# Kernel optimization log

Hardware: AMD Instinct MI355X
Metric: run time of the kernel (lower is better)

## Reference

```python
import jax, jax.numpy as jnp
import numpy as np

N_NODES = 10000
N_EDGES = 160000
D = 256
L = 2
EPS = 1e-5


def setup_inputs() -> dict:
    key = jax.random.key(0)
    ks = jax.random.split(key, 12)
    s = 0.05  # weight init scale to keep activations tame
    return {
        "node_h": jax.random.normal(ks[0], (N_NODES, D), jnp.float32),
        "edge_h": jax.random.normal(ks[1], (N_EDGES, D), jnp.float32),
        "src": jax.random.randint(ks[2], (N_EDGES,), 0, N_NODES, jnp.int32),
        "dst": jax.random.randint(ks[3], (N_EDGES,), 0, N_NODES, jnp.int32),
        "Kw": jax.random.normal(ks[4], (L, 2 * D, D), jnp.float32) * s,
        "Kb": jnp.zeros((L, D), jnp.float32),
        "Vw": jax.random.normal(ks[5], (L, 2 * D, D), jnp.float32) * s,
        "Vb": jnp.zeros((L, D), jnp.float32),
        "Qw": jax.random.normal(ks[6], (L, D, D), jnp.float32) * s,
        "Qb": jnp.zeros((L, D), jnp.float32),
        "Ww": jax.random.normal(ks[7], (L, 2 * D, D), jnp.float32) * s,
        "Wb": jnp.zeros((L, D), jnp.float32),
        "Ew": jax.random.normal(ks[8], (L, 3 * D, D), jnp.float32) * s,
        "Eb": jnp.zeros((L, D), jnp.float32),
        "ln_g": jnp.ones((D,), jnp.float32),
        "ln_b": jnp.zeros((D,), jnp.float32),
    }


def _layernorm(x, g, b):
    mu = jnp.mean(x, axis=-1, keepdims=True)
    var = jnp.mean(jnp.square(x - mu), axis=-1, keepdims=True)
    return (x - mu) * jax.lax.rsqrt(var + EPS) * g + b


def _hypergraph_layer(h_n, h_e, src, dst, Kw, Kb, Vw, Vb, Qw, Qb, Ww, Wb, Ew, Eb):
    n = h_n.shape[0]
    src_h = h_n[src]                                   # [E, D] gather
    msg = jnp.concatenate([src_h * h_e, src_h], axis=1)  # [E, 2D]
    Q = h_n @ Qw + Qb                                  # [N, D]
    K = msg @ Kw + Kb                                  # [E, D]
    V = msg @ Vw + Vb                                  # [E, D]
    alpha = Q[dst] * K                                 # v_mul_e -> [E, D]
    # edge_softmax: per-destination-node, per-feature softmax over edges
    m = jax.ops.segment_max(alpha, dst, num_segments=n)
    e = jnp.exp(alpha - m[dst])
    z = jax.ops.segment_sum(e, dst, num_segments=n)
    a = e / z[dst]
    agg = jax.ops.segment_sum(a * V, dst, num_segments=n)  # sum aggregation [N, D]
    h_n_new = jnp.concatenate([agg, h_n], axis=1) @ Ww + Wb
    h_e_new = jnp.concatenate([h_n_new[src], h_n_new[dst], h_e], axis=1) @ Ew + Eb
    return h_n_new, h_e_new


def reference(node_h, edge_h, src, dst, Kw, Kb, Vw, Vb, Qw, Qb, Ww, Wb, Ew, Eb, ln_g, ln_b):
    h_n, h_e = node_h, edge_h
    for l in range(L):  # small fixed layer count
        h_n, h_e = _hypergraph_layer(h_n, h_e, src, dst,
                                     Kw[l], Kb[l], Vw[l], Vb[l], Qw[l], Qb[l],
                                     Ww[l], Wb[l], Ew[l], Eb[l])
        # relu -> layernorm; dropout is identity in eval mode
        h_n = _layernorm(jax.nn.relu(h_n), ln_g, ln_b)
        h_e = _layernorm(jax.nn.relu(h_e), ln_g, ln_b)
    return h_n, h_e
```

## Files before the change

### kernel.cpp

```cpp
#include <hip/hip_runtime.h>

#define NN 10000
#define NE 160000
#define DD 256
#define LEPS 1e-5f

typedef __attribute__((ext_vector_type(8))) short short8v;
typedef __attribute__((ext_vector_type(4))) float floatx4;
typedef unsigned short US;

static __device__ __forceinline__ US f2bf(float f){
  unsigned u = __builtin_bit_cast(unsigned, f);
  u += 0x7FFFu + ((u >> 16) & 1u);
  return (US)(u >> 16);
}
static __device__ __forceinline__ float bf2f(US s){
  unsigned u = ((unsigned)s) << 16;
  return __builtin_bit_cast(float, u);
}
template<typename T>
static __device__ __forceinline__ void ld8(const T* p, float* o){
  if constexpr (sizeof(T) == 2) {
    union { US h[8]; uint4 q; } u;
    u.q = *(const uint4*)p;
#pragma unroll
    for (int j = 0; j < 8; ++j) o[j] = bf2f(u.h[j]);
  } else {
    float4 a = *(const float4*)p; float4 b = *(const float4*)(p + 4);
    o[0]=a.x; o[1]=a.y; o[2]=a.z; o[3]=a.w; o[4]=b.x; o[5]=b.y; o[6]=b.z; o[7]=b.w;
  }
}
template<typename OT>
static __device__ __forceinline__ void st1(OT* p, float v){
  if constexpr (sizeof(OT) == 2) *p = (OT)f2bf(v); else *p = (OT)v;
}

#define AOFF_Q  0
#define AOFF_K1 (32*2048)
#define AOFF_K2 (64*2048)
#define AOFF_V1 (96*2048)
#define AOFF_V2 (128*2048)
#define AOFF_W  (160*2048)
#define AOFF_E1 (224*2048)
#define AOFF_E2 (256*2048)
#define AOFF_E3 (288*2048)
__global__ void pack_all_k(const float* __restrict__ Qw, const float* __restrict__ Kw,
                           const float* __restrict__ Vw, const float* __restrict__ Ww,
                           const float* __restrict__ Ew, US* __restrict__ arena){
  int i = blockIdx.x * 256 + threadIdx.x;
  int g = i >> 8, n = i & 255;
  const float* src; int row0;
  if      (g <  32){ src = Qw; row0 = g*8; }
  else if (g <  64){ src = Kw; row0 = (g-32)*8; }
  else if (g <  96){ src = Kw; row0 = 256 + (g-64)*8; }
  else if (g < 128){ src = Vw; row0 = (g-96)*8; }
  else if (g < 160){ src = Vw; row0 = 256 + (g-128)*8; }
  else if (g < 224){ src = Ww; row0 = (g-160)*8; }
  else if (g < 256){ src = Ew; row0 = (g-224)*8; }
  else if (g < 288){ src = Ew; row0 = 256 + (g-256)*8; }
  else             { src = Ew; row0 = 512 + (g-288)*8; }
  union { US h[8]; uint4 q; } pk;
#pragma unroll
  for (int j = 0; j < 8; ++j) pk.h[j] = f2bf(src[(size_t)(row0 + j)*DD + n]);
  *(uint4*)(arena + (size_t)g*2048 + n*8) = pk.q;
}

template<typename AT, typename OT>
__global__ __launch_bounds__(256, 2)
void gemm_nmulti_k(const AT* __restrict__ p0,
                   const US* bp0, const float* b0, OT* o0,
                   const US* bp1, const float* b1, OT* o1,
                   const US* bp2, const float* b2, OT* o2, int M)
{
  const US* Bp  = (blockIdx.y == 0) ? bp0 : (blockIdx.y == 1 ? bp1 : bp2);
  const float* bias = (blockIdx.y == 0) ? b0 : (blockIdx.y == 1 ? b1 : b2);
  OT* out = (blockIdx.y == 0) ? o0 : (blockIdx.y == 1 ? o1 : o2);
  __shared__ __align__(16) US Alds[64][40];
  __shared__ __align__(16) US Blds[8192];
  const int tid  = threadIdx.x;
  const int lane = tid & 63;
  const int wav  = tid >> 6;
  const int bm   = blockIdx.x * 64;

  floatx4 acc[4][4];
#pragma unroll
  for (int i = 0; i < 4; ++i)
#pragma unroll
    for (int j = 0; j < 4; ++j) acc[i][j] = (floatx4){0.f,0.f,0.f,0.f};

  const int ar = tid >> 2;
  const int ak = (tid & 3) << 3;
  int grow = bm + ar; if (grow > M - 1) grow = M - 1;
  const AT* rA = p0 + (size_t)grow * DD;
  const int rq = lane >> 4;
  const int cl = lane & 15;

  for (int k0 = 0; k0 < 256; k0 += 32) {
    float av[8]; ld8(rA + k0 + ak, av);
    union { US h[8]; uint4 q; } pk;
#pragma unroll
    for (int j = 0; j < 8; ++j) pk.h[j] = f2bf(av[j]);
    *(uint4*)&Alds[ar][ak] = pk.q;

    const uint4* bsrc = (const uint4*)(Bp + (size_t)(k0 >> 3) * 2048);
    uint4* bdst = (uint4*)Blds;
#pragma unroll
    for (int u = 0; u < 4; ++u) bdst[tid + u*256] = bsrc[tid + u*256];
    __syncthreads();

    short8v af[4], bfr[4];
#pragma unroll
    for (int i = 0; i < 4; ++i) af[i] = *(const short8v*)&Alds[i*16 + cl][rq*8];
#pragma unroll
    for (int j = 0; j < 4; ++j) bfr[j] = *(const short8v*)&Blds[(size_t)(rq*256 + wav*64 + j*16 + cl) * 8];
#pragma unroll
    for (int i = 0; i < 4; ++i)
#pragma unroll
      for (int j = 0; j < 4; ++j)
        acc[i][j] = __builtin_amdgcn_mfma_f32_16x16x32_bf16(af[i], bfr[j], acc[i][j], 0, 0, 0);
    __syncthreads();
  }

#pragma unroll
  for (int i = 0; i < 4; ++i)
#pragma unroll
    for (int r = 0; r < 4; ++r) {
      int gm = bm + i*16 + rq*4 + r;
      if (gm < M) {
#pragma unroll
        for (int j = 0; j < 4; ++j) {
          int n = wav*64 + j*16 + cl;
          float b = bias ? bias[n] : 0.f;
          st1(out + (size_t)gm*DD + n, acc[i][j][r] + b);
        }
      }
    }
}

template<typename AT, typename OT>
__global__ __launch_bounds__(256, 2)
void gemm_w_k(const float* __restrict__ p0, const AT* __restrict__ p1,
              const US* __restrict__ Bp, const float* __restrict__ bias,
              const float* __restrict__ lg, const float* __restrict__ lb,
              float* __restrict__ Craw, OT* __restrict__ Cln, int M)
{
  __shared__ __align__(16) US Alds[64][40];
  __shared__ __align__(16) US Blds[8192];
  __shared__ float S1[4][64], S2[4][64];
  const int tid  = threadIdx.x;
  const int lane = tid & 63;
  const int wav  = tid >> 6;
  const int bm   = blockIdx.x * 64;

  floatx4 acc[4][4];
#pragma unroll
  for (int i = 0; i < 4; ++i)
#pragma unroll
    for (int j = 0; j < 4; ++j) acc[i][j] = (floatx4){0.f,0.f,0.f,0.f};

  const int ar = tid >> 2;
  const int ak = (tid & 3) << 3;
  int grow = bm + ar; if (grow > M - 1) grow = M - 1;
  const float* rA = p0 + (size_t)grow * DD;
  const AT*    rB = p1 + (size_t)grow * DD;
  const int rq = lane >> 4;
  const int cl = lane & 15;

  for (int k0 = 0; k0 < 512; k0 += 32) {
    const int kk = k0 + ak;
    float av[8];
    if (kk < DD) ld8(rA + kk, av); else ld8(rB + kk - DD, av);
    union { US h[8]; uint4 q; } pk;
#pragma unroll
    for (int j = 0; j < 8; ++j) pk.h[j] = f2bf(av[j]);
    *(uint4*)&Alds[ar][ak] = pk.q;

    const uint4* bsrc = (const uint4*)(Bp + (size_t)(k0 >> 3) * 2048);
    uint4* bdst = (uint4*)Blds;
#pragma unroll
    for (int u = 0; u < 4; ++u) bdst[tid + u*256] = bsrc[tid + u*256];
    __syncthreads();

    short8v af[4], bfr[4];
#pragma unroll
    for (int i = 0; i < 4; ++i) af[i] = *(const short8v*)&Alds[i*16 + cl][rq*8];
#pragma unroll
    for (int j = 0; j < 4; ++j) bfr[j] = *(const short8v*)&Blds[(size_t)(rq*256 + wav*64 + j*16 + cl) * 8];
#pragma unroll
    for (int i = 0; i < 4; ++i)
#pragma unroll
      for (int j = 0; j < 4; ++j)
        acc[i][j] = __builtin_amdgcn_mfma_f32_16x16x32_bf16(af[i], bfr[j], acc[i][j], 0, 0, 0);
    __syncthreads();
  }

#pragma unroll
  for (int i = 0; i < 4; ++i)
#pragma unroll
    for (int j = 0; j < 4; ++j) {
      int n = wav*64 + j*16 + cl;
      float bs = bias[n];
#pragma unroll
      for (int r = 0; r < 4; ++r) {
        int gm = bm + i*16 + rq*4 + r;
        float val = acc[i][j][r] + bs;
        if (gm < M) Craw[(size_t)gm*DD + n] = val;
        acc[i][j][r] = fmaxf(val, 0.f);
      }
    }
#pragma unroll
  for (int i = 0; i < 4; ++i)
#pragma unroll
    for (int r = 0; r < 4; ++r) {
      float s1 = 0.f, s2 = 0.f;
#pragma unroll
      for (int j = 0; j < 4; ++j){ float v = acc[i][j][r]; s1 += v; s2 += v*v; }
#pragma unroll
      for (int o = 1; o < 16; o <<= 1){ s1 += __shfl_xor(s1, o, 64); s2 += __shfl_xor(s2, o, 64); }
      if (cl == 0){ S1[wav][i*16 + rq*4 + r] = s1; S2[wav][i*16 + rq*4 + r] = s2; }
    }
  __syncthreads();
#pragma unroll
  for (int i = 0; i < 4; ++i)
#pragma unroll
    for (int r = 0; r < 4; ++r) {
      int rr = i*16 + rq*4 + r;
      float t1 = S1[0][rr] + S1[1][rr] + S1[2][rr] + S1[3][rr];
      float t2 = S2[0][rr] + S2[1][rr] + S2[2][rr] + S2[3][rr];
      float mu = t1 * (1.f/256.f);
      float var = t2 * (1.f/256.f) - mu*mu;
      float rs = rsqrtf(fmaxf(var, 0.f) + LEPS);
      int gm = bm + i*16 + rq*4 + r;
      if (gm < M) {
#pragma unroll
        for (int j = 0; j < 4; ++j) {
          int n = wav*64 + j*16 + cl;
          st1(Cln + (size_t)gm*DD + n, (acc[i][j][r] - mu) * rs * lg[n] + lb[n]);
        }
      }
    }
}

template<typename AT>
__global__ __launch_bounds__(256, 2)
void gemm_kve_k(const AT* __restrict__ p0, const AT* __restrict__ p1,
                const int* __restrict__ srcI,
                const US* __restrict__ BpK, const US* __restrict__ BpV,
                const US* __restrict__ KN, const US* __restrict__ VN,
                const int* __restrict__ eperm,
                US* __restrict__ Km, US* __restrict__ Vm, int M)
{
  __shared__ __align__(16) US Alds[64][40];
  __shared__ __align__(16) US BldsK[8192];
  __shared__ __align__(16) US BldsV[8192];
  const int tid  = threadIdx.x;
  const int lane = tid & 63;
  const int wav  = tid >> 6;
  const int bm   = blockIdx.x * 64;

  floatx4 accK[4][4], accV[4][4];
#pragma unroll
  for (int i = 0; i < 4; ++i)
#pragma unroll
    for (int j = 0; j < 4; ++j){ accK[i][j] = (floatx4){0.f,0.f,0.f,0.f}; accV[i][j] = (floatx4){0.f,0.f,0.f,0.f}; }

  const int ar = tid >> 2;
  const int ak = (tid & 3) << 3;
  int grow = bm + ar; if (grow > M - 1) grow = M - 1;
  int s = srcI[grow];
  const AT* rA = p0 + (size_t)s * DD;
  const AT* rB = p1 + (size_t)grow * DD;
  const int rq = lane >> 4;
  const int cl = lane & 15;

  for (int k0 = 0; k0 < 256; k0 += 32) {
    const int kk = k0 + ak;
    float av[8], bv[8];
    ld8(rA + kk, av); ld8(rB + kk, bv);
    union { US h[8]; uint4 q; } pk;
#pragma unroll
    for (int j = 0; j < 8; ++j) pk.h[j] = f2bf(av[j] * bv[j]);
    *(uint4*)&Alds[ar][ak] = pk.q;

    const uint4* bsK = (const uint4*)(BpK + (size_t)(k0 >> 3) * 2048);
    const uint4* bsV = (const uint4*)(BpV + (size_t)(k0 >> 3) * 2048);
    uint4* bdK = (uint4*)BldsK; uint4* bdV = (uint4*)BldsV;
#pragma unroll
    for (int u = 0; u < 4; ++u){ bdK[tid + u*256] = bsK[tid + u*256]; bdV[tid + u*256] = bsV[tid + u*256]; }
    __syncthreads();

    short8v af[4], bK4[4], bV4[4];
#pragma unroll
    for (int i = 0; i < 4; ++i) af[i] = *(const short8v*)&Alds[i*16 + cl][rq*8];
#pragma unroll
    for (int j = 0; j < 4; ++j){
      size_t bi = (size_t)(rq*256 + wav*64 + j*16 + cl) * 8;
      bK4[j] = *(const short8v*)&BldsK[bi];
      bV4[j] = *(const short8v*)&BldsV[bi];
    }
#pragma unroll
    for (int i = 0; i < 4; ++i)
#pragma unroll
      for (int j = 0; j < 4; ++j){
        accK[i][j] = __builtin_amdgcn_mfma_f32_16x16x32_bf16(af[i], bK4[j], accK[i][j], 0, 0, 0);
        accV[i][j] = __builtin_amdgcn_mfma_f32_16x16x32_bf16(af[i], bV4[j], accV[i][j], 0, 0, 0);
      }
    __syncthreads();
  }

#pragma unroll
  for (int i = 0; i < 4; ++i)
#pragma unroll
    for (int r = 0; r < 4; ++r) {
      int gm = bm + i*16 + rq*4 + r;
      if (gm < M) {
        int pg = eperm[gm];
        int sg = srcI[gm];
        const US* kn = KN + (size_t)sg * DD;
        const US* vn = VN + (size_t)sg * DD;
#pragma unroll
        for (int j = 0; j < 4; ++j) {
          int n = wav*64 + j*16 + cl;
          Km[(size_t)pg*DD + n] = f2bf(accK[i][j][r] + bf2f(kn[n]));
          Vm[(size_t)pg*DD + n] = f2bf(accV[i][j][r] + bf2f(vn[n]));
        }
      }
    }
}

template<typename AT, typename OT>
__global__ __launch_bounds__(256, 2)
void gemm_e_k(const AT* __restrict__ he, const int* __restrict__ srcI,
              const int* __restrict__ dstI, const US* __restrict__ Bp,
              const US* __restrict__ EN1, const US* __restrict__ EN2,
              const float* __restrict__ lg, const float* __restrict__ lb,
              OT* __restrict__ Cln, int M)
{
  __shared__ __align__(16) US Alds[64][40];
  __shared__ __align__(16) US Blds[8192];
  __shared__ float S1[4][64], S2[4][64];
  const int tid  = threadIdx.x;
  const int lane = tid & 63;
  const int wav  = tid >> 6;
  const int bm   = blockIdx.x * 64;

  floatx4 acc[4][4];
#pragma unroll
  for (int i = 0; i < 4; ++i)
#pragma unroll
    for (int j = 0; j < 4; ++j) acc[i][j] = (floatx4){0.f,0.f,0.f,0.f};

  const int ar = tid >> 2;
  const int ak = (tid & 3) << 3;
  int grow = bm + ar; if (grow > M - 1) grow = M - 1;
  const AT* rA = he + (size_t)grow * DD;
  const int rq = lane >> 4;
  const int cl = lane & 15;

  for (int k0 = 0; k0 < 256; k0 += 32) {
    float av[8]; ld8(rA + k0 + ak, av);
    union { US h[8]; uint4 q; } pk;
#pragma unroll
    for (int j = 0; j < 8; ++j) pk.h[j] = f2bf(av[j]);
    *(uint4*)&Alds[ar][ak] = pk.q;

    const uint4* bsrc = (const uint4*)(Bp + (size_t)(k0 >> 3) * 2048);
    uint4* bdst = (uint4*)Blds;
#pragma unroll
    for (int u = 0; u < 4; ++u) bdst[tid + u*256] = bsrc[tid + u*256];
    __syncthreads();

    short8v af[4], bfr[4];
#pragma unroll
    for (int i = 0; i < 4; ++i) af[i] = *(const short8v*)&Alds[i*16 + cl][rq*8];
#pragma unroll
    for (int j = 0; j < 4; ++j) bfr[j] = *(const short8v*)&Blds[(size_t)(rq*256 + wav*64 + j*16 + cl) * 8];
#pragma unroll
    for (int i = 0; i < 4; ++i)
#pragma unroll
      for (int j = 0; j < 4; ++j)
        acc[i][j] = __builtin_amdgcn_mfma_f32_16x16x32_bf16(af[i], bfr[j], acc[i][j], 0, 0, 0);
    __syncthreads();
  }

#pragma unroll
  for (int i = 0; i < 4; ++i)
#pragma unroll
    for (int r = 0; r < 4; ++r) {
      int gm = bm + i*16 + rq*4 + r;
      int gmc = (gm < M) ? gm : (M - 1);
      const US* e1 = EN1 + (size_t)srcI[gmc] * DD;
      const US* e2 = EN2 + (size_t)dstI[gmc] * DD;
#pragma unroll
      for (int j = 0; j < 4; ++j) {
        int n = wav*64 + j*16 + cl;
        float val = acc[i][j][r] + bf2f(e1[n]) + bf2f(e2[n]);
        acc[i][j][r] = fmaxf(val, 0.f);
      }
    }
#pragma unroll
  for (int i = 0; i < 4; ++i)
#pragma unroll
    for (int r = 0; r < 4; ++r) {
      float s1 = 0.f, s2 = 0.f;
#pragma unroll
      for (int j = 0; j < 4; ++j){ float v = acc[i][j][r]; s1 += v; s2 += v*v; }
#pragma unroll
      for (int o = 1; o < 16; o <<= 1){ s1 += __shfl_xor(s1, o, 64); s2 += __shfl_xor(s2, o, 64); }
      if (cl == 0){ S1[wav][i*16 + rq*4 + r] = s1; S2[wav][i*16 + rq*4 + r] = s2; }
    }
  __syncthreads();
#pragma unroll
  for (int i = 0; i < 4; ++i)
#pragma unroll
    for (int r = 0; r < 4; ++r) {
      int rr = i*16 + rq*4 + r;
      float t1 = S1[0][rr] + S1[1][rr] + S1[2][rr] + S1[3][rr];
      float t2 = S2[0][rr] + S2[1][rr] + S2[2][rr] + S2[3][rr];
      float mu = t1 * (1.f/256.f);
      float var = t2 * (1.f/256.f) - mu*mu;
      float rs = rsqrtf(fmaxf(var, 0.f) + LEPS);
      int gm = bm + i*16 + rq*4 + r;
      if (gm < M) {
#pragma unroll
        for (int j = 0; j < 4; ++j) {
          int n = wav*64 + j*16 + cl;
          st1(Cln + (size_t)gm*DD + n, (acc[i][j][r] - mu) * rs * lg[n] + lb[n]);
        }
      }
    }
}

__global__ void count_k(const int* __restrict__ dst, int* __restrict__ cnt, int e){
  int i = blockIdx.x * blockDim.x + threadIdx.x;
  if (i < e) atomicAdd(&cnt[dst[i]], 1);
}
__global__ void scan_k(const int* __restrict__ cnt, int* __restrict__ rp, int n){
  __shared__ int part[256];
  const int t = threadIdx.x;
  const int chunk = (n + 255) / 256;
  int lo = t * chunk, hi = lo + chunk; if (hi > n) hi = n; if (lo > n) lo = n;
  int s = 0;
  for (int i = lo; i < hi; ++i) s += cnt[i];
  part[t] = s; __syncthreads();
  if (t == 0){ int run = 0; for (int i = 0; i < 256; ++i){ int tmp = part[i]; part[i] = run; run += tmp; } rp[n] = run; }
  __syncthreads();
  int run = part[t];
  for (int i = lo; i < hi; ++i){ rp[i] = run; run += cnt[i]; }
}
__global__ void scatter_k(const int* __restrict__ dst, const int* __restrict__ rp,
                          int* __restrict__ pos, int* __restrict__ eperm, int e){
  int i = blockIdx.x * blockDim.x + threadIdx.x;
  if (i >= e) return;
  int d = dst[i];
  int p = atomicAdd(&pos[d], 1);
  eperm[i] = rp[d] + p;
}

__global__ __launch_bounds__(256)
void node_agg_k(const int* __restrict__ rp,
                const float* __restrict__ Q, const US* __restrict__ Km,
                const US* __restrict__ Vm, float* __restrict__ agg)
{
  int d = blockIdx.x, f = threadIdx.x;
  int beg = rp[d], end = rp[d + 1];
  float q = Q[(size_t)d * DD + f];
  float m = -3.0e38f, z = 0.f, s = 0.f;
  for (int i = beg; i < end; ++i){
    float a  = q * bf2f(Km[(size_t)i * DD + f]);
    float vv = bf2f(Vm[(size_t)i * DD + f]);
    float mn = fmaxf(m, a);
    float sc = __expf(m - mn);
    float w  = __expf(a - mn);
    z = z * sc + w;
    s = s * sc + w * vv;
    m = mn;
  }
  agg[(size_t)d * DD + f] = (z > 0.f) ? (s / z) : 0.f;
}

__global__ void sentinel_k(int hostbits, float* out){
  int code = 0;
  if (hostbits & 1) code = 1;
  else if (hostbits & 2) code = 2;
  else if (hostbits & 4) code = 3;
  else if (hostbits & 8) code = 4;
  if (code) out[0] = (float)code * 1.0e6f;
}

struct Bufs {
  float *Q, *agg, *hn_new;
  US *KN, *VN, *EN1, *EN2, *Kmat, *Vmat, *arena;
  int *rp, *eperm;
  const int *src, *dst;
  const float *lg, *lb;
};
template<typename AT, typename OT>
static void layer_run(const Bufs& B, const AT* hn_in, const AT* he_in,
                      OT* hn_out, OT* he_out,
                      const float* Kb, const float* Vb, const float* Qb,
                      const float* Wb, const float* Eb, hipStream_t stream)
{
  const int gN = (NN + 63) / 64, gE = (NE + 63) / 64;
  gemm_nmulti_k<AT, float><<<dim3(gN, 1), 256, 0, stream>>>(hn_in,
      B.arena + AOFF_Q, Qb, B.Q,  B.arena + AOFF_Q, Qb, B.Q,  B.arena + AOFF_Q, Qb, B.Q, NN);
  gemm_nmulti_k<AT, US><<<dim3(gN, 2), 256, 0, stream>>>(hn_in,
      B.arena + AOFF_K2, Kb, B.KN,  B.arena + AOFF_V2, Vb, B.VN,  B.arena + AOFF_V2, Vb, B.VN, NN);
  gemm_kve_k<AT><<<gE, 256, 0, stream>>>(hn_in, he_in, B.src,
      B.arena + AOFF_K1, B.arena + AOFF_V1, B.KN, B.VN, B.eperm, B.Kmat, B.Vmat, NE);
  node_agg_k<<<NN, 256, 0, stream>>>(B.rp, B.Q, B.Kmat, B.Vmat, B.agg);
  gemm_w_k<AT, OT><<<gN, 256, 0, stream>>>(B.agg, hn_in, B.arena + AOFF_W, Wb,
      B.lg, B.lb, B.hn_new, hn_out, NN);
  gemm_nmulti_k<float, US><<<dim3(gN, 2), 256, 0, stream>>>(B.hn_new,
      B.arena + AOFF_E1, Eb, B.EN1,  B.arena + AOFF_E2, nullptr, B.EN2,
      B.arena + AOFF_E2, nullptr, B.EN2, NN);
  gemm_e_k<AT, OT><<<gE, 256, 0, stream>>>(he_in, B.src, B.dst, B.arena + AOFF_E3,
      B.EN1, B.EN2, B.lg, B.lb, he_out, NE);
}

extern "C" void kernel_launch(void* const* d_in, const int* in_sizes, int n_in,
                              void* d_out, int out_size, void* d_ws, size_t ws_size,
                              hipStream_t stream) {
  const float* node_h = (const float*)d_in[0];
  const float* edge_h = (const float*)d_in[1];
  const int*   src    = (const int*)d_in[2];
  const int*   dst    = (const int*)d_in[3];
  const float* Kw = (const float*)d_in[4];  const float* Kb = (const float*)d_in[5];
  const float* Vw = (const float*)d_in[6];  const float* Vb = (const float*)d_in[7];
  const float* Qw = (const float*)d_in[8];  const float* Qb = (const float*)d_in[9];
  const float* Ww = (const float*)d_in[10]; const float* Wb = (const float*)d_in[11];
  const float* Ew = (const float*)d_in[12]; const float* Eb = (const float*)d_in[13];
  const float* ln_g = (const float*)d_in[14];
  const float* ln_b = (const float*)d_in[15];

  char* w = (char*)d_ws; size_t off = 0;
  auto alloc = [&](size_t bytes)->char* {
    char* p = w + off; off += (bytes + 255) & ~(size_t)255; return p;
  };
  float* Q      = (float*)alloc((size_t)NN * DD * 4);
  float* agg    = (float*)alloc((size_t)NN * DD * 4);
  float* hn_new = (float*)alloc((size_t)NN * DD * 4);
  US* hn_cur = (US*)alloc((size_t)NN * DD * 2);
  US* KN     = (US*)alloc((size_t)NN * DD * 2);
  US* VN     = (US*)alloc((size_t)NN * DD * 2);
  US* EN1    = (US*)alloc((size_t)NN * DD * 2);
  US* EN2    = (US*)alloc((size_t)NN * DD * 2);
  US* Kmat   = (US*)alloc((size_t)NE * DD * 2);
  US* Vmat   = (US*)alloc((size_t)NE * DD * 2);
  US* he_cur = (US*)alloc((size_t)NE * DD * 2);
  US* arena  = (US*)alloc((size_t)320 * 2048 * 2);
  int* cnt   = (int*)alloc((size_t)NN * 4);
  int* rp    = (int*)alloc((size_t)(NN + 1) * 4);
  int* pos   = (int*)alloc((size_t)NN * 4);
  int* eperm = (int*)alloc((size_t)NE * 4);

  float* out_hn = (float*)d_out;
  float* out_he = out_hn + (size_t)NN * DD;

  int hostbits = 0;
  {
    static const int exp_sizes[16] = {NN*DD, NE*DD, NE, NE, 2*512*DD, 2*DD, 2*512*DD, 2*DD,
                                      2*DD*DD, 2*DD, 2*512*DD, 2*DD, 2*768*DD, 2*DD, DD, DD};
    if (n_in != 16) hostbits |= 2;
    else { for (int i = 0; i < 16; ++i) if (in_sizes[i] != exp_sizes[i]) hostbits |= 2; }
    if (out_size != NN*DD + NE*DD) hostbits |= 4;
    if (off > ws_size) hostbits |= 1;
  }
  if (hostbits) {
    sentinel_k<<<1, 1, 0, stream>>>(hostbits, out_hn);
    return;
  }

  hipMemsetAsync(cnt, 0, (size_t)NN * 4, stream);
  hipMemsetAsync(pos, 0, (size_t)NN * 4, stream);
  count_k<<<(NE + 255)/256, 256, 0, stream>>>(dst, cnt, NE);
  scan_k<<<1, 256, 0, stream>>>(cnt, rp, NN);
  scatter_k<<<(NE + 255)/256, 256, 0, stream>>>(dst, rp, pos, eperm, NE);

  Bufs B{Q, agg, hn_new, KN, VN, EN1, EN2, Kmat, Vmat, arena, rp, eperm, src, dst, ln_g, ln_b};

  pack_all_k<<<320, 256, 0, stream>>>(Qw, Kw, Vw, Ww, Ew, arena);
  layer_run<float, US>(B, node_h, edge_h, hn_cur, he_cur,
                       Kb, Vb, Qb, Wb, Eb, stream);
  pack_all_k<<<320, 256, 0, stream>>>(Qw + (size_t)256*DD, Kw + (size_t)512*DD,
                                      Vw + (size_t)512*DD, Ww + (size_t)512*DD,
                                      Ew + (size_t)768*DD, arena);
  layer_run<US, float>(B, hn_cur, he_cur, out_hn, out_he,
                       Kb + DD, Vb + DD, Qb + DD, Wb + DD, Eb + DD, stream);

  if (hipGetLastError() != hipSuccess) {
    sentinel_k<<<1, 1, 0, stream>>>(8, out_hn);
  }
}
```

Baseline: 865.8 us.

## Preload A rows into registers before GEMM loops and merge Q into bf16 multi-GEMM

Each GEMM kernel now issues all global loads for its A-row slice up front, converting them to bf16 and keeping them in registers, instead of loading inside each k-step. This lets the memory latency overlap rather than stall each iteration, at the cost of extra registers per thread. Q is also computed as bf16 in the same launch as the node-side K/V projections, removing one launch and halving Q traffic into node_agg_k. Holding Q in bf16 adds some rounding error to the attention logits.

```diff
diff --git a/kernel.cpp b/kernel.cpp
--- a/kernel.cpp
+++ b/kernel.cpp
@@ -33,6 +33,12 @@
 template<typename OT>
 static __device__ __forceinline__ void st1(OT* p, float v){
   if constexpr (sizeof(OT) == 2) *p = (OT)f2bf(v); else *p = (OT)v;
+}
+static __device__ __forceinline__ uint4 pack8(const float* a){
+  union { US h[8]; uint4 q; } pk;
+#pragma unroll
+  for (int j = 0; j < 8; ++j) pk.h[j] = f2bf(a[j]);
+  return pk.q;
 }
 
 #define AOFF_Q  0
@@ -95,14 +101,16 @@
   const int rq = lane >> 4;
   const int cl = lane & 15;
 
-  for (int k0 = 0; k0 < 256; k0 += 32) {
-    float av[8]; ld8(rA + k0 + ak, av);
-    union { US h[8]; uint4 q; } pk;
-#pragma unroll
-    for (int j = 0; j < 8; ++j) pk.h[j] = f2bf(av[j]);
-    *(uint4*)&Alds[ar][ak] = pk.q;
-
-    const uint4* bsrc = (const uint4*)(Bp + (size_t)(k0 >> 3) * 2048);
+  uint4 arow[8];
+#pragma unroll
+  for (int t = 0; t < 8; ++t) {
+    float av[8]; ld8(rA + t*32 + ak, av);
+    arow[t] = pack8(av);
+  }
+
+  for (int t = 0; t < 8; ++t) {
+    *(uint4*)&Alds[ar][ak] = arow[t];
+    const uint4* bsrc = (const uint4*)(Bp + (size_t)(t*4) * 2048);
     uint4* bdst = (uint4*)Blds;
 #pragma unroll
     for (int u = 0; u < 4; ++u) bdst[tid + u*256] = bsrc[tid + u*256];
@@ -166,16 +174,18 @@
   const int rq = lane >> 4;
   const int cl = lane & 15;
 
-  for (int k0 = 0; k0 < 512; k0 += 32) {
-    const int kk = k0 + ak;
+  uint4 arow[16];
+#pragma unroll
+  for (int t = 0; t < 16; ++t) {
+    const int kk = t*32 + ak;
     float av[8];
     if (kk < DD) ld8(rA + kk, av); else ld8(rB + kk - DD, av);
-    union { US h[8]; uint4 q; } pk;
-#pragma unroll
-    for (int j = 0; j < 8; ++j) pk.h[j] = f2bf(av[j]);
-    *(uint4*)&Alds[ar][ak] = pk.q;
-
-    const uint4* bsrc = (const uint4*)(Bp + (size_t)(k0 >> 3) * 2048);
+    arow[t] = pack8(av);
+  }
+
+  for (int t = 0; t < 16; ++t) {
+    *(uint4*)&Alds[ar][ak] = arow[t];
+    const uint4* bsrc = (const uint4*)(Bp + (size_t)(t*4) * 2048);
     uint4* bdst = (uint4*)Blds;
 #pragma unroll
     for (int u = 0; u < 4; ++u) bdst[tid + u*256] = bsrc[tid + u*256];
@@ -273,17 +283,22 @@
   const int rq = lane >> 4;
   const int cl = lane & 15;
 
-  for (int k0 = 0; k0 < 256; k0 += 32) {
-    const int kk = k0 + ak;
+  uint4 msg[8];
+#pragma unroll
+  for (int t = 0; t < 8; ++t) {
+    const int kk = t*32 + ak;
     float av[8], bv[8];
     ld8(rA + kk, av); ld8(rB + kk, bv);
-    union { US h[8]; uint4 q; } pk;
-#pragma unroll
-    for (int j = 0; j < 8; ++j) pk.h[j] = f2bf(av[j] * bv[j]);
-    *(uint4*)&Alds[ar][ak] = pk.q;
-
-    const uint4* bsK = (const uint4*)(BpK + (size_t)(k0 >> 3) * 2048);
-    const uint4* bsV = (const uint4*)(BpV + (size_t)(k0 >> 3) * 2048);
+    float mv[8];
+#pragma unroll
+    for (int j = 0; j < 8; ++j) mv[j] = av[j] * bv[j];
+    msg[t] = pack8(mv);
+  }
+
+  for (int t = 0; t < 8; ++t) {
+    *(uint4*)&Alds[ar][ak] = msg[t];
+    const uint4* bsK = (const uint4*)(BpK + (size_t)(t*4) * 2048);
+    const uint4* bsV = (const uint4*)(BpV + (size_t)(t*4) * 2048);
     uint4* bdK = (uint4*)BldsK; uint4* bdV = (uint4*)BldsV;
 #pragma unroll
     for (int u = 0; u < 4; ++u){ bdK[tid + u*256] = bsK[tid + u*256]; bdV[tid + u*256] = bsV[tid + u*256]; }
@@ -357,14 +372,16 @@
   const int rq = lane >> 4;
   const int cl = lane & 15;
 
-  for (int k0 = 0; k0 < 256; k0 += 32) {
-    float av[8]; ld8(rA + k0 + ak, av);
-    union { US h[8]; uint4 q; } pk;
-#pragma unroll
-    for (int j = 0; j < 8; ++j) pk.h[j] = f2bf(av[j]);
-    *(uint4*)&Alds[ar][ak] = pk.q;
-
-    const uint4* bsrc = (const uint4*)(Bp + (size_t)(k0 >> 3) * 2048);
+  uint4 arow[8];
+#pragma unroll
+  for (int t = 0; t < 8; ++t) {
+    float av[8]; ld8(rA + t*32 + ak, av);
+    arow[t] = pack8(av);
+  }
+
+  for (int t = 0; t < 8; ++t) {
+    *(uint4*)&Alds[ar][ak] = arow[t];
+    const uint4* bsrc = (const uint4*)(Bp + (size_t)(t*4) * 2048);
     uint4* bdst = (uint4*)Blds;
 #pragma unroll
     for (int u = 0; u < 4; ++u) bdst[tid + u*256] = bsrc[tid + u*256];
@@ -459,12 +476,12 @@
 
 __global__ __launch_bounds__(256)
 void node_agg_k(const int* __restrict__ rp,
-                const float* __restrict__ Q, const US* __restrict__ Km,
+                const US* __restrict__ Q, const US* __restrict__ Km,
                 const US* __restrict__ Vm, float* __restrict__ agg)
 {
   int d = blockIdx.x, f = threadIdx.x;
   int beg = rp[d], end = rp[d + 1];
-  float q = Q[(size_t)d * DD + f];
+  float q = bf2f(Q[(size_t)d * DD + f]);
   float m = -3.0e38f, z = 0.f, s = 0.f;
   for (int i = beg; i < end; ++i){
     float a  = q * bf2f(Km[(size_t)i * DD + f]);
@@ -489,8 +506,8 @@
 }
 
 struct Bufs {
-  float *Q, *agg, *hn_new;
-  US *KN, *VN, *EN1, *EN2, *Kmat, *Vmat, *arena;
+  float *agg, *hn_new;
+  US *QN, *KN, *VN, *EN1, *EN2, *Kmat, *Vmat, *arena;
   int *rp, *eperm;
   const int *src, *dst;
   const float *lg, *lb;
@@ -502,13 +519,13 @@
                       const float* Wb, const float* Eb, hipStream_t stream)
 {
   const int gN = (NN + 63) / 64, gE = (NE + 63) / 64;
-  gemm_nmulti_k<AT, float><<<dim3(gN, 1), 256, 0, stream>>>(hn_in,
-      B.arena + AOFF_Q, Qb, B.Q,  B.arena + AOFF_Q, Qb, B.Q,  B.arena + AOFF_Q, Qb, B.Q, NN);
-  gemm_nmulti_k<AT, US><<<dim3(gN, 2), 256, 0, stream>>>(hn_in,
-      B.arena + AOFF_K2, Kb, B.KN,  B.arena + AOFF_V2, Vb, B.VN,  B.arena + AOFF_V2, Vb, B.VN, NN);
+  gemm_nmulti_k<AT, US><<<dim3(gN, 3), 256, 0, stream>>>(hn_in,
+      B.arena + AOFF_Q, Qb, B.QN,
+      B.arena + AOFF_K2, Kb, B.KN,
+      B.arena + AOFF_V2, Vb, B.VN, NN);
   gemm_kve_k<AT><<<gE, 256, 0, stream>>>(hn_in, he_in, B.src,
       B.arena + AOFF_K1, B.arena + AOFF_V1, B.KN, B.VN, B.eperm, B.Kmat, B.Vmat, NE);
-  node_agg_k<<<NN, 256, 0, stream>>>(B.rp, B.Q, B.Kmat, B.Vmat, B.agg);
+  node_agg_k<<<NN, 256, 0, stream>>>(B.rp, B.QN, B.Kmat, B.Vmat, B.agg);
   gemm_w_k<AT, OT><<<gN, 256, 0, stream>>>(B.agg, hn_in, B.arena + AOFF_W, Wb,
       B.lg, B.lb, B.hn_new, hn_out, NN);
   gemm_nmulti_k<float, US><<<dim3(gN, 2), 256, 0, stream>>>(B.hn_new,
@@ -537,9 +554,9 @@
   auto alloc = [&](size_t bytes)->char* {
     char* p = w + off; off += (bytes + 255) & ~(size_t)255; return p;
   };
-  float* Q      = (float*)alloc((size_t)NN * DD * 4);
   float* agg    = (float*)alloc((size_t)NN * DD * 4);
   float* hn_new = (float*)alloc((size_t)NN * DD * 4);
+  US* QN     = (US*)alloc((size_t)NN * DD * 2);
   US* hn_cur = (US*)alloc((size_t)NN * DD * 2);
   US* KN     = (US*)alloc((size_t)NN * DD * 2);
   US* VN     = (US*)alloc((size_t)NN * DD * 2);
@@ -577,7 +594,7 @@
   scan_k<<<1, 256, 0, stream>>>(cnt, rp, NN);
   scatter_k<<<(NE + 255)/256, 256, 0, stream>>>(dst, rp, pos, eperm, NE);
 
-  Bufs B{Q, agg, hn_new, KN, VN, EN1, EN2, Kmat, Vmat, arena, rp, eperm, src, dst, ln_g, ln_b};
+  Bufs B{agg, hn_new, QN, KN, VN, EN1, EN2, Kmat, Vmat, arena, rp, eperm, src, dst, ln_g, ln_b};
 
   pack_all_k<<<320, 256, 0, stream>>>(Qw, Kw, Vw, Ww, Ew, arena);
   layer_run<float, US>(B, node_h, edge_h, hn_cur, he_cur,
```

After: 901.3 us. 4.1% more time.
